# Performance work log

Measured on AMD Instinct MI355X. Metric: run time of the kernel, lower is better.

Reference implementation:

```python
import jax, jax.numpy as jnp
import numpy as np

N_QUBITS = 6
EPS = 1e-5
B = 65536


def _ry(t):
    # RY(t) = [[cos t/2, -sin t/2], [sin t/2, cos t/2]]; t scalar or (B,)
    c = jnp.cos(0.5 * t)
    s = jnp.sin(0.5 * t)
    row0 = jnp.stack([c, -s], -1)
    row1 = jnp.stack([s, c], -1)
    return jnp.stack([row0, row1], -2).astype(jnp.complex64)


def _rz(t):
    # RZ(t) = diag(e^{-it/2}, e^{it/2})
    e = jnp.exp(-0.5j * t)
    z = jnp.zeros_like(e)
    row0 = jnp.stack([e, z], -1)
    row1 = jnp.stack([z, jnp.conj(e)], -1)
    return jnp.stack([row0, row1], -2)


def _apply_1q(psi, U, w):
    # psi: (B, 2,...,2); U: (2,2) shared or (B,2,2) batched
    psi = jnp.moveaxis(psi, w + 1, -1)
    if U.ndim == 2:
        psi = psi @ U.T
    else:
        psi = jnp.einsum('b...i,bji->b...j', psi, U)
    return jnp.moveaxis(psi, -1, w + 1)


def _cnot(psi, c, t):
    ca, ta = c + 1, t + 1
    p0 = jnp.take(psi, 0, axis=ca)
    p1 = jnp.take(psi, 1, axis=ca)
    p1 = jnp.flip(p1, axis=ta - 1 if ta > ca else ta)  # X on target where control=1
    return jnp.stack([p0, p1], axis=ca)


def _sel(psi, theta):
    # StronglyEntanglingLayers: Rot(phi, th, om) per wire, then ring of CNOTs with range r
    n_layers = theta.shape[0]
    for l in range(n_layers):
        for w in range(N_QUBITS):
            phi, th, om = theta[l, w, 0], theta[l, w, 1], theta[l, w, 2]
            U = _rz(om) @ _ry(th) @ _rz(phi)  # Rot = RZ(om) RY(th) RZ(phi)
            psi = _apply_1q(psi, U, w)
        r = l % (N_QUBITS - 1) + 1  # PennyLane default ranges
        for w in range(N_QUBITS):
            psi = _cnot(psi, w, (w + r) % N_QUBITS)
    return psi


def setup_inputs() -> dict:
    key = jax.random.key(0)
    ks = jax.random.split(key, 11)
    d = 64
    return {
        'x': jax.random.normal(ks[0], (B, d), jnp.float32),
        'W1': jax.random.normal(ks[1], (64, d), jnp.float32) / np.sqrt(d),
        'b1': jax.random.normal(ks[2], (64,), jnp.float32) * 0.01,
        'ln_g': jnp.ones((64,), jnp.float32),
        'ln_b': jnp.zeros((64,), jnp.float32),
        'W2': jax.random.normal(ks[3], (N_QUBITS, 64), jnp.float32) / 8.0,
        'b2': jax.random.normal(ks[4], (N_QUBITS,), jnp.float32) * 0.01,
        'theta_shared': jax.random.uniform(ks[5], (2, N_QUBITS, 3), jnp.float32, 0.0, 2.0 * np.pi),
        'theta_task': jax.random.uniform(ks[6], (1, N_QUBITS, 3), jnp.float32, 0.0, 2.0 * np.pi),
        'Wc': jax.random.normal(ks[7], (5, N_QUBITS), jnp.float32) / np.sqrt(N_QUBITS),
        'bc': jnp.zeros((5,), jnp.float32),
    }


def reference(x, W1, b1, ln_g, ln_b, W2, b2, theta_shared, theta_task, Wc, bc):
    # encoder: Linear -> ReLU -> LayerNorm -> Linear -> Tanh
    h = jax.nn.relu(x @ W1.T + b1)
    mu = jnp.mean(h, -1, keepdims=True)
    var = jnp.mean((h - mu) ** 2, -1, keepdims=True)
    h = (h - mu) * jax.lax.rsqrt(var + EPS) * ln_g + ln_b
    z = jnp.tanh(h @ W2.T + b2)  # (B, 6)

    # batched 6-qubit state-vector simulator
    n = z.shape[0]
    psi = jnp.zeros((n, 2 ** N_QUBITS), jnp.complex64).at[:, 0].set(1.0)
    psi = psi.reshape((n,) + (2,) * N_QUBITS)
    ang = np.pi * z
    for w in range(N_QUBITS):
        psi = _apply_1q(psi, _ry(ang[:, w]), w)  # batched RY encoding
    psi = _sel(psi, theta_shared)
    psi = _sel(psi, theta_task)

    probs = psi.real ** 2 + psi.imag ** 2  # (n, 2,...,2)
    zvals = []
    for w in range(N_QUBITS):
        pw = jnp.moveaxis(probs, w + 1, 1).reshape(n, 2, -1).sum(-1)
        zvals.append(pw[:, 0] - pw[:, 1])  # <Z_w>
    q = jnp.stack(zvals, -1)  # (n, 6)
    return q @ Wc.T + bc
```

## Files before the change

kernel.cpp:

```cpp
#include <hip/hip_runtime.h>
#include <math.h>

#define NQ 6
#define DIM 64
#define W1S 65
#define PI_F 3.14159265358979323846f

template <int CTRL, int ROWM, bool BC>
__device__ __forceinline__ float dpp_add_src(float v) {
  int r = __builtin_amdgcn_update_dpp(0, __float_as_int(v), CTRL, ROWM, 0xF, BC);
  return __int_as_float(r);
}

__device__ __forceinline__ float red_sum(float v) {
  v += dpp_add_src<0x111, 0xF, true>(v);
  v += dpp_add_src<0x112, 0xF, true>(v);
  v += dpp_add_src<0x114, 0xF, true>(v);
  v += dpp_add_src<0x118, 0xF, true>(v);
  v += dpp_add_src<0x142, 0xA, false>(v);
  v += dpp_add_src<0x143, 0xC, false>(v);
  return v;
}
__device__ __forceinline__ float bcast63(float v) {
  return __int_as_float(__builtin_amdgcn_readlane(__float_as_int(v), 63));
}
__device__ __forceinline__ float rdlane(float v, int l) {
  return __int_as_float(__builtin_amdgcn_readlane(__float_as_int(v), l));
}

template <int W>
__device__ __forceinline__ float sh_partner(float v) {
  if constexpr (W == 5) {
    int i = __float_as_int(v);
    return __int_as_float(__builtin_amdgcn_update_dpp(i, i, 0xB1, 0xF, 0xF, false));
  } else if constexpr (W == 4) {
    int i = __float_as_int(v);
    return __int_as_float(__builtin_amdgcn_update_dpp(i, i, 0x4E, 0xF, 0xF, false));
  } else if constexpr (W == 3) {
    return __int_as_float(__builtin_amdgcn_ds_swizzle(__float_as_int(v), 0x101F));
  } else if constexpr (W == 2) {
    return __int_as_float(__builtin_amdgcn_ds_swizzle(__float_as_int(v), 0x201F));
  } else if constexpr (W == 1) {
    return __int_as_float(__builtin_amdgcn_ds_swizzle(__float_as_int(v), 0x401F));
  } else {
    return __shfl_xor(v, 32, 64);
  }
}

template <int W>
__device__ __forceinline__ void gate_w(float& re, float& im, float4 c, int lane) {
  float pr = sh_partner<W>(re);
  float pi = sh_partner<W>(im);
  const bool hi = (lane & (32 >> W)) != 0;
  float sa = hi ? -c.y : c.y;
  float sb = hi ? -c.z : c.z;
  float nr = c.x * re;
  nr = fmaf(-sa, im, nr);
  nr = fmaf(sb, pr, nr);
  nr = fmaf(-c.w, pi, nr);
  float ni = c.x * im;
  ni = fmaf(sa, re, ni);
  ni = fmaf(sb, pi, ni);
  ni = fmaf(c.w, pr, ni);
  re = nr; im = ni;
}

__device__ __forceinline__ int cnot_src(int j, int r) {
  int i = j;
  #pragma unroll
  for (int w = 5; w >= 0; --w) {
    const int cm = 32 >> w;
    const int tm = 32 >> ((w + r) % NQ);
    if (i & cm) i ^= tm;
  }
  return i;
}

__global__ __launch_bounds__(256) void qmaml_v9(
    const float* __restrict__ x,
    const float* __restrict__ W1,
    const float* __restrict__ b1,
    const float* __restrict__ ln_g,
    const float* __restrict__ ln_b,
    const float* __restrict__ W2,
    const float* __restrict__ b2,
    const float* __restrict__ th_sh,
    const float* __restrict__ th_tk,
    const float* __restrict__ Wc,
    const float* __restrict__ bc,
    float* __restrict__ out,
    int B)
{
  __shared__ float w1t[64 * W1S];
  __shared__ float4 coef[18];

  const int tid = threadIdx.x;

  #pragma unroll
  for (int it = 0; it < 16; ++it) {
    const int idx = tid + it * 256;
    w1t[(idx & 63) * W1S + (idx >> 6)] = W1[idx];
  }
  if (tid < 18) {
    const int layer = tid / 6, w = tid % 6;
    const float* th = (layer < 2) ? (th_sh + (layer * 6 + w) * 3)
                                  : (th_tk + w * 3);
    const float phi = th[0], the = th[1], om = th[2];
    float S, C;   sincosf(0.5f * the,        &S,  &C);
    float sS, cS; sincosf(0.5f * (om + phi), &sS, &cS);
    float sD, cD; sincosf(0.5f * (om - phi), &sD, &cD);
    coef[tid] = make_float4(C * cS, -C * sS, -S * cD, S * sD);
  }
  __syncthreads();

  const int lane = tid & 63;
  const int wid = __builtin_amdgcn_readfirstlane(blockIdx.x * 4 + (tid >> 6));
  const int nw = gridDim.x * 4;

  const float b1v = b1[lane];
  const float lgv = ln_g[lane];
  const float lbv = ln_b[lane];
  float w2v[NQ];
  #pragma unroll
  for (int m = 0; m < NQ; ++m) w2v[m] = W2[m * DIM + lane];
  const float b2v = (lane < NQ) ? b2[lane] : 0.0f;
  const float bcv = (lane < 5) ? bc[lane] : 0.0f;
  float g5[5];
  #pragma unroll
  for (int j = 0; j < 5; ++j) {
    float a = 0.0f;
    #pragma unroll
    for (int w = 0; w < NQ; ++w) {
      const float wc = Wc[j * NQ + w];
      a += (lane & (32 >> w)) ? -wc : wc;
    }
    g5[j] = a;
  }
  const int pa1 = cnot_src(lane, 1) << 2;
  const int pa2 = cnot_src(lane, 2) << 2;

  for (int t = wid; t < B; t += nw) {
    const float* __restrict__ xr =
        x + (size_t)__builtin_amdgcn_readfirstlane(t) * DIM;

    float a0 = b1v, a1 = 0.0f, a2 = 0.0f, a3 = 0.0f;
    #pragma unroll
    for (int k = 0; k < DIM; k += 4) {
      a0 = fmaf(w1t[(k + 0) * W1S + lane], xr[k + 0], a0);
      a1 = fmaf(w1t[(k + 1) * W1S + lane], xr[k + 1], a1);
      a2 = fmaf(w1t[(k + 2) * W1S + lane], xr[k + 2], a2);
      a3 = fmaf(w1t[(k + 3) * W1S + lane], xr[k + 3], a3);
    }
    float h = fmaxf((a0 + a1) + (a2 + a3), 0.0f);

    const float s1 = bcast63(red_sum(h)) * (1.0f / DIM);
    const float s2 = bcast63(red_sum(h * h)) * (1.0f / DIM);
    const float rs = __builtin_amdgcn_rsqf(s2 - s1 * s1 + 1e-5f);
    h = fmaf((h - s1) * rs, lgv, lbv);

    float y = 0.0f;
    #pragma unroll
    for (int m = 0; m < NQ; ++m) {
      const float r = bcast63(red_sum(w2v[m] * h));
      y = (lane == m) ? r : y;
    }
    y += b2v;

    float4 k0 = coef[0], k1 = coef[1], k2 = coef[2],
           k3 = coef[3], k4 = coef[4], k5 = coef[5];

    const float e = __expf(2.0f * y);
    const float tz = fmaf(-2.0f, __builtin_amdgcn_rcpf(e + 1.0f), 1.0f);
    const float ha = (0.5f * PI_F) * tz;
    const float sv = __sinf(ha);
    const float cv = __cosf(ha);

    float re = (lane & 32) ? rdlane(sv, 0) : rdlane(cv, 0);
    re *= (lane & 16) ? rdlane(sv, 1) : rdlane(cv, 1);
    re *= (lane &  8) ? rdlane(sv, 2) : rdlane(cv, 2);
    re *= (lane &  4) ? rdlane(sv, 3) : rdlane(cv, 3);
    re *= (lane &  2) ? rdlane(sv, 4) : rdlane(cv, 4);
    re *= (lane &  1) ? rdlane(sv, 5) : rdlane(cv, 5);
    float im = 0.0f;

    gate_w<0>(re, im, k0, lane);  k0 = coef[6];
    gate_w<1>(re, im, k1, lane);  k1 = coef[7];
    gate_w<2>(re, im, k2, lane);  k2 = coef[8];
    gate_w<3>(re, im, k3, lane);  k3 = coef[9];
    gate_w<4>(re, im, k4, lane);  k4 = coef[10];
    gate_w<5>(re, im, k5, lane);  k5 = coef[11];
    re = __int_as_float(__builtin_amdgcn_ds_bpermute(pa1, __float_as_int(re)));
    im = __int_as_float(__builtin_amdgcn_ds_bpermute(pa1, __float_as_int(im)));

    gate_w<0>(re, im, k0, lane);  k0 = coef[12];
    gate_w<1>(re, im, k1, lane);  k1 = coef[13];
    gate_w<2>(re, im, k2, lane);  k2 = coef[14];
    gate_w<3>(re, im, k3, lane);  k3 = coef[15];
    gate_w<4>(re, im, k4, lane);  k4 = coef[16];
    gate_w<5>(re, im, k5, lane);  k5 = coef[17];
    re = __int_as_float(__builtin_amdgcn_ds_bpermute(pa2, __float_as_int(re)));
    im = __int_as_float(__builtin_amdgcn_ds_bpermute(pa2, __float_as_int(im)));

    gate_w<0>(re, im, k0, lane);
    gate_w<1>(re, im, k1, lane);
    gate_w<2>(re, im, k2, lane);
    gate_w<3>(re, im, k3, lane);
    gate_w<4>(re, im, k4, lane);
    gate_w<5>(re, im, k5, lane);
    re = __int_as_float(__builtin_amdgcn_ds_bpermute(pa1, __float_as_int(re)));
    im = __int_as_float(__builtin_amdgcn_ds_bpermute(pa1, __float_as_int(im)));

    const float p = fmaf(re, re, im * im);
    float o0 = bcast63(red_sum(p * g5[0]));
    float o1 = bcast63(red_sum(p * g5[1]));
    float o2 = bcast63(red_sum(p * g5[2]));
    float o3 = bcast63(red_sum(p * g5[3]));
    float o4 = bcast63(red_sum(p * g5[4]));
    float vout = (lane == 0) ? o0 :
                 (lane == 1) ? o1 :
                 (lane == 2) ? o2 :
                 (lane == 3) ? o3 : o4;
    if (lane < 5) out[(size_t)t * 5 + lane] = vout + bcv;
  }
}

extern "C" void kernel_launch(void* const* d_in, const int* in_sizes, int n_in,
                              void* d_out, int out_size, void* d_ws, size_t ws_size,
                              hipStream_t stream) {
  const float* x     = (const float*)d_in[0];
  const float* W1    = (const float*)d_in[1];
  const float* b1    = (const float*)d_in[2];
  const float* ln_g  = (const float*)d_in[3];
  const float* ln_b  = (const float*)d_in[4];
  const float* W2    = (const float*)d_in[5];
  const float* b2    = (const float*)d_in[6];
  const float* th_sh = (const float*)d_in[7];
  const float* th_tk = (const float*)d_in[8];
  const float* Wc    = (const float*)d_in[9];
  const float* bc    = (const float*)d_in[10];
  float* out = (float*)d_out;

  const int B = in_sizes[0] / DIM;
  int blocks = (B + 3) / 4;
  if (blocks > 2048) blocks = 2048;
  qmaml_v9<<<blocks, 256, 0, stream>>>(x, W1, b1, ln_g, ln_b, W2, b2,
                                       th_sh, th_tk, Wc, bc, out, B);
}
```

Baseline: 66.53 us.

## Precompute fixed 64x64 circuit unitary and apply it as a matrix-vector product

A new pre-kernel simulates the theta-only part of the circuit (the SEL layers and CNOT rings) once per basis column and builds the full 64x64 complex unitary in workspace. The main kernel loads this unitary into LDS and replaces the 18 per-sample gate applications and permutes with a real-vector-times-complex-matrix product over LDS, taking advantage of the encoded state being real. This removes per-sample cross-lane shuffle chains but adds 64 LDS float2 reads per sample, a 32 KB LDS footprint that may reduce occupancy, and an extra kernel launch. The grid cap is also lowered.

Measured after the change: 127.2 us. 1.91x slower.

```diff
diff --git a/kernel.cpp b/kernel.cpp
--- a/kernel.cpp
+++ b/kernel.cpp
@@ -26,6 +26,9 @@
 }
 __device__ __forceinline__ float rdlane(float v, int l) {
   return __int_as_float(__builtin_amdgcn_readlane(__float_as_int(v), l));
+}
+__device__ __forceinline__ float bperm(int pa, float v) {
+  return __int_as_float(__builtin_amdgcn_ds_bpermute(pa, __float_as_int(v)));
 }
 
 template <int W>
@@ -76,31 +79,13 @@
   return i;
 }
 
-__global__ __launch_bounds__(256) void qmaml_v9(
-    const float* __restrict__ x,
-    const float* __restrict__ W1,
-    const float* __restrict__ b1,
-    const float* __restrict__ ln_g,
-    const float* __restrict__ ln_b,
-    const float* __restrict__ W2,
-    const float* __restrict__ b2,
+__global__ __launch_bounds__(256) void build_u(
     const float* __restrict__ th_sh,
     const float* __restrict__ th_tk,
-    const float* __restrict__ Wc,
-    const float* __restrict__ bc,
-    float* __restrict__ out,
-    int B)
+    float2* __restrict__ uout)
 {
-  __shared__ float w1t[64 * W1S];
   __shared__ float4 coef[18];
-
   const int tid = threadIdx.x;
-
-  #pragma unroll
-  for (int it = 0; it < 16; ++it) {
-    const int idx = tid + it * 256;
-    w1t[(idx & 63) * W1S + (idx >> 6)] = W1[idx];
-  }
   if (tid < 18) {
     const int layer = tid / 6, w = tid % 6;
     const float* th = (layer < 2) ? (th_sh + (layer * 6 + w) * 3)
@@ -114,7 +99,75 @@
   __syncthreads();
 
   const int lane = tid & 63;
-  const int wid = __builtin_amdgcn_readfirstlane(blockIdx.x * 4 + (tid >> 6));
+  const int col = blockIdx.x * 4 + (tid >> 6);
+  const int pa1 = cnot_src(lane, 1) << 2;
+  const int pa2 = cnot_src(lane, 2) << 2;
+
+  float re = (lane == col) ? 1.0f : 0.0f;
+  float im = 0.0f;
+
+  gate_w<0>(re, im, coef[0], lane);
+  gate_w<1>(re, im, coef[1], lane);
+  gate_w<2>(re, im, coef[2], lane);
+  gate_w<3>(re, im, coef[3], lane);
+  gate_w<4>(re, im, coef[4], lane);
+  gate_w<5>(re, im, coef[5], lane);
+  re = bperm(pa1, re); im = bperm(pa1, im);
+
+  gate_w<0>(re, im, coef[6], lane);
+  gate_w<1>(re, im, coef[7], lane);
+  gate_w<2>(re, im, coef[8], lane);
+  gate_w<3>(re, im, coef[9], lane);
+  gate_w<4>(re, im, coef[10], lane);
+  gate_w<5>(re, im, coef[11], lane);
+  re = bperm(pa2, re); im = bperm(pa2, im);
+
+  gate_w<0>(re, im, coef[12], lane);
+  gate_w<1>(re, im, coef[13], lane);
+  gate_w<2>(re, im, coef[14], lane);
+  gate_w<3>(re, im, coef[15], lane);
+  gate_w<4>(re, im, coef[16], lane);
+  gate_w<5>(re, im, coef[17], lane);
+  re = bperm(pa1, re); im = bperm(pa1, im);
+
+  uout[col * 64 + lane] = make_float2(re, im);
+}
+
+__global__ __launch_bounds__(256) void qmaml_v10(
+    const float* __restrict__ x,
+    const float* __restrict__ W1,
+    const float* __restrict__ b1,
+    const float* __restrict__ ln_g,
+    const float* __restrict__ ln_b,
+    const float* __restrict__ W2,
+    const float* __restrict__ b2,
+    const float* __restrict__ Wc,
+    const float* __restrict__ bc,
+    const float2* __restrict__ uglob,
+    float* __restrict__ out,
+    int B)
+{
+  __shared__ float w1t[64 * W1S];
+  __shared__ float2 uld[4096];
+  __shared__ float psiw[4][64];
+
+  const int tid = threadIdx.x;
+
+  #pragma unroll
+  for (int it = 0; it < 16; ++it) {
+    const int idx = tid + it * 256;
+    w1t[(idx & 63) * W1S + (idx >> 6)] = W1[idx];
+  }
+  #pragma unroll
+  for (int it = 0; it < 16; ++it) {
+    const int idx = tid + it * 256;
+    uld[idx] = uglob[idx];
+  }
+  __syncthreads();
+
+  const int lane = tid & 63;
+  const int wv = tid >> 6;
+  const int wid = __builtin_amdgcn_readfirstlane(blockIdx.x * 4 + wv);
   const int nw = gridDim.x * 4;
 
   const float b1v = b1[lane];
@@ -136,8 +189,6 @@
     }
     g5[j] = a;
   }
-  const int pa1 = cnot_src(lane, 1) << 2;
-  const int pa2 = cnot_src(lane, 2) << 2;
 
   for (int t = wid; t < B; t += nw) {
     const float* __restrict__ xr =
@@ -166,51 +217,39 @@
     }
     y += b2v;
 
-    float4 k0 = coef[0], k1 = coef[1], k2 = coef[2],
-           k3 = coef[3], k4 = coef[4], k5 = coef[5];
-
     const float e = __expf(2.0f * y);
     const float tz = fmaf(-2.0f, __builtin_amdgcn_rcpf(e + 1.0f), 1.0f);
     const float ha = (0.5f * PI_F) * tz;
     const float sv = __sinf(ha);
     const float cv = __cosf(ha);
 
-    float re = (lane & 32) ? rdlane(sv, 0) : rdlane(cv, 0);
-    re *= (lane & 16) ? rdlane(sv, 1) : rdlane(cv, 1);
-    re *= (lane &  8) ? rdlane(sv, 2) : rdlane(cv, 2);
-    re *= (lane &  4) ? rdlane(sv, 3) : rdlane(cv, 3);
-    re *= (lane &  2) ? rdlane(sv, 4) : rdlane(cv, 4);
-    re *= (lane &  1) ? rdlane(sv, 5) : rdlane(cv, 5);
-    float im = 0.0f;
-
-    gate_w<0>(re, im, k0, lane);  k0 = coef[6];
-    gate_w<1>(re, im, k1, lane);  k1 = coef[7];
-    gate_w<2>(re, im, k2, lane);  k2 = coef[8];
-    gate_w<3>(re, im, k3, lane);  k3 = coef[9];
-    gate_w<4>(re, im, k4, lane);  k4 = coef[10];
-    gate_w<5>(re, im, k5, lane);  k5 = coef[11];
-    re = __int_as_float(__builtin_amdgcn_ds_bpermute(pa1, __float_as_int(re)));
-    im = __int_as_float(__builtin_amdgcn_ds_bpermute(pa1, __float_as_int(im)));
-
-    gate_w<0>(re, im, k0, lane);  k0 = coef[12];
-    gate_w<1>(re, im, k1, lane);  k1 = coef[13];
-    gate_w<2>(re, im, k2, lane);  k2 = coef[14];
-    gate_w<3>(re, im, k3, lane);  k3 = coef[15];
-    gate_w<4>(re, im, k4, lane);  k4 = coef[16];
-    gate_w<5>(re, im, k5, lane);  k5 = coef[17];
-    re = __int_as_float(__builtin_amdgcn_ds_bpermute(pa2, __float_as_int(re)));
-    im = __int_as_float(__builtin_amdgcn_ds_bpermute(pa2, __float_as_int(im)));
-
-    gate_w<0>(re, im, k0, lane);
-    gate_w<1>(re, im, k1, lane);
-    gate_w<2>(re, im, k2, lane);
-    gate_w<3>(re, im, k3, lane);
-    gate_w<4>(re, im, k4, lane);
-    gate_w<5>(re, im, k5, lane);
-    re = __int_as_float(__builtin_amdgcn_ds_bpermute(pa1, __float_as_int(re)));
-    im = __int_as_float(__builtin_amdgcn_ds_bpermute(pa1, __float_as_int(im)));
-
-    const float p = fmaf(re, re, im * im);
+    float a = (lane & 32) ? rdlane(sv, 0) : rdlane(cv, 0);
+    a *= (lane & 16) ? rdlane(sv, 1) : rdlane(cv, 1);
+    a *= (lane &  8) ? rdlane(sv, 2) : rdlane(cv, 2);
+    a *= (lane &  4) ? rdlane(sv, 3) : rdlane(cv, 3);
+    a *= (lane &  2) ? rdlane(sv, 4) : rdlane(cv, 4);
+    a *= (lane &  1) ? rdlane(sv, 5) : rdlane(cv, 5);
+    psiw[wv][lane] = a;
+    asm volatile("s_waitcnt lgkmcnt(0)" ::: "memory");
+
+    float r0 = 0.f, r1 = 0.f, r2 = 0.f, r3 = 0.f;
+    float i0 = 0.f, i1 = 0.f, i2 = 0.f, i3 = 0.f;
+    #pragma unroll
+    for (int k4 = 0; k4 < 16; ++k4) {
+      const float4 p4 = reinterpret_cast<const float4*>(psiw[wv])[k4];
+      const float2 u0 = uld[(4 * k4 + 0) * 64 + lane];
+      const float2 u1 = uld[(4 * k4 + 1) * 64 + lane];
+      const float2 u2 = uld[(4 * k4 + 2) * 64 + lane];
+      const float2 u3 = uld[(4 * k4 + 3) * 64 + lane];
+      r0 = fmaf(u0.x, p4.x, r0);  i0 = fmaf(u0.y, p4.x, i0);
+      r1 = fmaf(u1.x, p4.y, r1);  i1 = fmaf(u1.y, p4.y, i1);
+      r2 = fmaf(u2.x, p4.z, r2);  i2 = fmaf(u2.y, p4.z, i2);
+      r3 = fmaf(u3.x, p4.w, r3);  i3 = fmaf(u3.y, p4.w, i3);
+    }
+    const float rr = (r0 + r1) + (r2 + r3);
+    const float ii = (i0 + i1) + (i2 + i3);
+
+    const float p = fmaf(rr, rr, ii * ii);
     float o0 = bcast63(red_sum(p * g5[0]));
     float o1 = bcast63(red_sum(p * g5[1]));
     float o2 = bcast63(red_sum(p * g5[2]));
@@ -239,10 +278,14 @@
   const float* Wc    = (const float*)d_in[9];
   const float* bc    = (const float*)d_in[10];
   float* out = (float*)d_out;
+  float2* u = (float2*)d_ws;
 
   const int B = in_sizes[0] / DIM;
+
+  build_u<<<16, 256, 0, stream>>>(th_sh, th_tk, u);
+
   int blocks = (B + 3) / 4;
-  if (blocks > 2048) blocks = 2048;
-  qmaml_v9<<<blocks, 256, 0, stream>>>(x, W1, b1, ln_g, ln_b, W2, b2,
-                                       th_sh, th_tk, Wc, bc, out, B);
-}
+  if (blocks > 768) blocks = 768;
+  qmaml_v10<<<blocks, 256, 0, stream>>>(x, W1, b1, ln_g, ln_b, W2, b2,
+                                        Wc, bc, u, out, B);
+}
```
